# Performance work log

Hardware: AMD Instinct MI355X
Metric: run time of the kernel (lower is better)

The kernel has to match this reference:

```python
import jax, jax.numpy as jnp
import numpy as np

B, S, D, H = 4, 2048, 512, 8
EPS = 1e-5

def _layer_norm(x, gamma, beta):
    mu = jnp.mean(x, axis=-1, keepdims=True)
    var = jnp.mean(jnp.square(x - mu), axis=-1, keepdims=True)
    return (x - mu) * jax.lax.rsqrt(var + EPS) * gamma + beta

def setup_inputs() -> dict:
    key = jax.random.key(0)
    ks = jax.random.split(key, 6)
    sc = 1.0 / np.sqrt(D)
    return {
        "seq_k": jax.random.normal(ks[0], (B, S, D), jnp.float32),
        "seq_q": jax.random.normal(ks[1], (B, S, D), jnp.float32),
        "seq_v": jax.random.normal(ks[2], (B, S, D), jnp.float32),
        "W1": jax.random.normal(ks[3], (D, D), jnp.float32) * sc,
        "W2": jax.random.normal(ks[4], (D, D), jnp.float32) * sc,
        "W3": jax.random.normal(ks[5], (D, D), jnp.float32) * sc,
        "gamma": jnp.ones((D,), jnp.float32),
        "beta": jnp.zeros((D,), jnp.float32),
    }

def reference(seq_k, seq_q, seq_v, W1, W2, W3, gamma, beta):
    # is_layer_norm=True: pre-LN on values; seq_v_value is the normed v
    v_in = _layer_norm(seq_v, gamma, beta)
    # nn.Linear(bias=False): y = x @ W^T
    q = seq_q @ W1.T
    k = seq_k @ W2.T
    v = v_in @ W3.T
    hd = D // H
    q = q.reshape(B, S, H, hd).transpose(0, 2, 1, 3)  # b h s d
    k = k.reshape(B, S, H, hd).transpose(0, 2, 1, 3)
    v = v.reshape(B, S, H, hd).transpose(0, 2, 1, 3)
    # faithful quirk: scores = K @ Q^T, unscaled
    scores = jnp.einsum("bhid,bhjd->bhij", k, q)  # b h s s
    attn = jax.nn.softmax(scores, axis=-1)
    out = jnp.einsum("bhij,bhjd->bhid", attn, v)  # b h s d
    out = out.transpose(0, 2, 1, 3).reshape(B, S, D)
    out = out + v_in                 # is_residual=True
    return _layer_norm(out, gamma, beta)  # final LN
```

## Files before the change

### kernel.cpp

```cpp
#include <hip/hip_runtime.h>
#include <math.h>

#define BB 4
#define SS 2048
#define DD 512
#define HH 8
#define HD 64
#define NTOK (BB*SS)
#define EPS 1e-5f

typedef _Float16 half8v __attribute__((ext_vector_type(8)));
typedef _Float16 half4v __attribute__((ext_vector_type(4)));
typedef _Float16 half2v __attribute__((ext_vector_type(2)));
typedef float f32x4 __attribute__((ext_vector_type(4)));

__device__ __forceinline__ void gload_lds16(const void* g, void* l) {
    __builtin_amdgcn_global_load_lds(
        (const __attribute__((address_space(1))) unsigned int*)g,
        (__attribute__((address_space(3))) unsigned int*)l, 16, 0, 0);
}

__global__ __launch_bounds__(256) void ln_kernel(const float* __restrict__ x,
                                                 const float* __restrict__ res,
                                                 const float* __restrict__ gamma,
                                                 const float* __restrict__ beta,
                                                 float* __restrict__ y,
                                                 _Float16* __restrict__ y16) {
    int row = blockIdx.x;
    const float* xr = x + (size_t)row * DD;
    int t = threadIdx.x;
    float2 v = ((const float2*)xr)[t];
    if (res) {
        float2 r = ((const float2*)(res + (size_t)row * DD))[t];
        v.x += r.x; v.y += r.y;
    }
    float s = v.x + v.y;
    float ss = v.x * v.x + v.y * v.y;
    #pragma unroll
    for (int off = 32; off; off >>= 1) {
        s  += __shfl_down(s,  off);
        ss += __shfl_down(ss, off);
    }
    __shared__ float ws0[4], ws1[4];
    int wid = t >> 6, lane = t & 63;
    if (lane == 0) { ws0[wid] = s; ws1[wid] = ss; }
    __syncthreads();
    __shared__ float mu_s, rstd_s;
    if (t == 0) {
        float S0 = ws0[0] + ws0[1] + ws0[2] + ws0[3];
        float S1 = ws1[0] + ws1[1] + ws1[2] + ws1[3];
        float mu = S0 * (1.0f / DD);
        float var = S1 * (1.0f / DD) - mu * mu;
        mu_s = mu;
        rstd_s = rsqrtf(var + EPS);
    }
    __syncthreads();
    float mu = mu_s, rstd = rstd_s;
    float2 g = ((const float2*)gamma)[t];
    float2 bb = ((const float2*)beta)[t];
    float2 o;
    o.x = (v.x - mu) * rstd * g.x + bb.x;
    o.y = (v.y - mu) * rstd * g.y + bb.y;
    if (y)   ((float2*)(y + (size_t)row * DD))[t] = o;
    if (y16) {
        half2v ho; ho[0] = (_Float16)o.x; ho[1] = (_Float16)o.y;
        *(half2v*)&y16[(size_t)row * DD + 2 * t] = ho;
    }
}

__global__ __launch_bounds__(256) void cast_f2h(const float* __restrict__ src,
                                                _Float16* __restrict__ dst) {
    size_t i = ((size_t)blockIdx.x * 256 + threadIdx.x) * 4;
    float4 v = *(const float4*)(src + i);
    half4v o;
    o[0] = (_Float16)v.x; o[1] = (_Float16)v.y;
    o[2] = (_Float16)v.z; o[3] = (_Float16)v.w;
    *(half4v*)(dst + i) = o;
}

#define GBM 128
#define GBN 128
#define GBK 64
__global__ __launch_bounds__(256) void gemm_mfma(const _Float16* __restrict__ Aall,
                                                 const _Float16* __restrict__ Wall,
                                                 _Float16* __restrict__ Call) {
    __shared__ __align__(16) _Float16 As[GBM * GBK];
    __shared__ __align__(16) _Float16 Ws[GBN * GBK];
    int z = blockIdx.z;
    const _Float16* A = Aall + (size_t)z * NTOK * DD;
    const _Float16* W = Wall + (size_t)z * DD * DD;
    _Float16* C = Call + (size_t)z * NTOK * DD;
    int t = threadIdx.x, w = t >> 6, lane = t & 63, q = lane >> 4, ln = lane & 15;
    int lrow = lane >> 3, lseg = lane & 7;
    int m0 = blockIdx.y * GBM, n0 = blockIdx.x * GBN;
    int wm = w & 1, wn = w >> 1;
    f32x4 acc[4][4];
    #pragma unroll
    for (int mt = 0; mt < 4; ++mt)
        #pragma unroll
        for (int nt = 0; nt < 4; ++nt)
            acc[mt][nt] = (f32x4){0.f, 0.f, 0.f, 0.f};

    int gs = lseg ^ lrow;
    for (int k0 = 0; k0 < DD; k0 += GBK) {
        #pragma unroll
        for (int p = 0; p < 4; ++p) {
            int r = w * 32 + p * 8 + lrow;
            gload_lds16(A + (size_t)(m0 + r) * DD + k0 + gs * 8,
                        As + (size_t)(w * 32 + p * 8) * GBK);
            gload_lds16(W + (size_t)(n0 + r) * DD + k0 + gs * 8,
                        Ws + (size_t)(w * 32 + p * 8) * GBK);
        }
        __syncthreads();
        #pragma unroll
        for (int kk = 0; kk < 2; ++kk) {
            int ch = ((4 * kk + q) ^ (ln & 7)) * 8;
            half8v af[4], wf[4];
            #pragma unroll
            for (int mt = 0; mt < 4; ++mt)
                af[mt] = *(half8v*)&As[(wm * 64 + mt * 16 + ln) * GBK + ch];
            #pragma unroll
            for (int nt = 0; nt < 4; ++nt)
                wf[nt] = *(half8v*)&Ws[(wn * 64 + nt * 16 + ln) * GBK + ch];
            #pragma unroll
            for (int mt = 0; mt < 4; ++mt)
                #pragma unroll
                for (int nt = 0; nt < 4; ++nt)
                    acc[mt][nt] = __builtin_amdgcn_mfma_f32_16x16x32_f16(
                        af[mt], wf[nt], acc[mt][nt], 0, 0, 0);
        }
        __syncthreads();
    }
    #pragma unroll
    for (int mt = 0; mt < 4; ++mt) {
        int mbase = m0 + wm * 64 + mt * 16 + q * 4;
        #pragma unroll
        for (int nt = 0; nt < 4; ++nt) {
            int n = n0 + wn * 64 + nt * 16 + ln;
            int h = n >> 6, d = n & 63;
            #pragma unroll
            for (int r = 0; r < 4; ++r) {
                int m = mbase + r;
                int b = m >> 11, s = m & (SS - 1);
                C[(((size_t)(b * HH + h) * SS + s) * HD) + d] = (_Float16)acc[mt][nt][r];
            }
        }
    }
}

__global__ __launch_bounds__(256) void transpose_v(const _Float16* __restrict__ vh,
                                                   _Float16* __restrict__ vt) {
    __shared__ __align__(16) _Float16 tile[64 * 72];
    int t = threadIdx.x;
    int s0 = blockIdx.x * 64;
    int bh = blockIdx.y;
    const _Float16* src = vh + ((size_t)bh * SS) * HD;
    _Float16* dst = vt + ((size_t)bh * HD) * SS;
    #pragma unroll
    for (int p = 0; p < 2; ++p) {
        int idx = t + 256 * p;
        int r = idx >> 3, seg = idx & 7;
        *(half8v*)&tile[r * 72 + seg * 8] =
            *(const half8v*)&src[(size_t)(s0 + r) * HD + seg * 8];
    }
    __syncthreads();
    #pragma unroll
    for (int p = 0; p < 2; ++p) {
        int idx = t + 256 * p;
        int d = idx >> 3, seg = idx & 7;
        half8v o;
        #pragma unroll
        for (int e = 0; e < 8; ++e) o[e] = tile[(seg * 8 + e) * 72 + d];
        *(half8v*)&dst[(size_t)d * SS + s0 + seg * 8] = o;
    }
}

#define AI 128
#define AJ 64
#define PLD 72
__global__ __launch_bounds__(256) void attn_mfma(const _Float16* __restrict__ qh,
                                                 const _Float16* __restrict__ kh,
                                                 const _Float16* __restrict__ vt,
                                                 float* __restrict__ out) {
    __shared__ __align__(16) _Float16 Qt[AJ * HD];
    __shared__ __align__(16) _Float16 Vs[HD * AJ];
    __shared__ __align__(16) _Float16 Ps[8 * 16 * PLD];
    int t = threadIdx.x, w = t >> 6, lane = t & 63, q = lane >> 4, ln = lane & 15;
    int lrow = lane >> 3, lseg = lane & 7;
    int i0 = blockIdx.x * AI;
    int bh = blockIdx.y, b = bh >> 3, h = bh & 7;
    const _Float16* Kb = kh + (size_t)bh * SS * HD;
    const _Float16* Qb = qh + (size_t)bh * SS * HD;
    const _Float16* Vb = vt + (size_t)bh * HD * SS;

    half8v kf[2][2];
    #pragma unroll
    for (int nt = 0; nt < 2; ++nt)
        #pragma unroll
        for (int kk = 0; kk < 2; ++kk)
            kf[nt][kk] = *(const half8v*)&Kb[(size_t)(i0 + w * 32 + nt * 16 + ln) * HD
                                             + kk * 32 + q * 8];

    f32x4 oacc[4][2];
    float m_run[2], l_run[2];
    #pragma unroll
    for (int nt = 0; nt < 2; ++nt) {
        m_run[nt] = -3.0e38f;
        l_run[nt] = 0.f;
        #pragma unroll
        for (int mtd = 0; mtd < 4; ++mtd) oacc[mtd][nt] = (f32x4){0.f, 0.f, 0.f, 0.f};
    }

    int gs = lseg ^ lrow;
    for (int j0 = 0; j0 < SS; j0 += AJ) {
        #pragma unroll
        for (int p = 0; p < 2; ++p) {
            int r = w * 16 + p * 8 + lrow;
            gload_lds16(Qb + (size_t)(j0 + r) * HD + gs * 8,
                        Qt + (size_t)(w * 16 + p * 8) * HD);
            gload_lds16(Vb + (size_t)r * SS + j0 + gs * 8,
                        Vs + (size_t)(w * 16 + p * 8) * AJ);
        }
        __syncthreads();

        f32x4 sacc[4][2];
        #pragma unroll
        for (int mt = 0; mt < 4; ++mt)
            #pragma unroll
            for (int nt = 0; nt < 2; ++nt)
                sacc[mt][nt] = (f32x4){0.f, 0.f, 0.f, 0.f};
        #pragma unroll
        for (int kk = 0; kk < 2; ++kk) {
            int ch = ((4 * kk + q) ^ (ln & 7)) * 8;
            half8v qf[4];
            #pragma unroll
            for (int mt = 0; mt < 4; ++mt)
                qf[mt] = *(half8v*)&Qt[(mt * 16 + ln) * HD + ch];
            #pragma unroll
            for (int mt = 0; mt < 4; ++mt)
                #pragma unroll
                for (int nt = 0; nt < 2; ++nt)
                    sacc[mt][nt] = __builtin_amdgcn_mfma_f32_16x16x32_f16(
                        qf[mt], kf[nt][kk], sacc[mt][nt], 0, 0, 0);
        }

        #pragma unroll
        for (int nt = 0; nt < 2; ++nt) {
            float mx = -3.0e38f;
            #pragma unroll
            for (int mt = 0; mt < 4; ++mt)
                #pragma unroll
                for (int r = 0; r < 4; ++r) mx = fmaxf(mx, sacc[mt][nt][r]);
            mx = fmaxf(mx, __shfl_xor(mx, 16));
            mx = fmaxf(mx, __shfl_xor(mx, 32));
            float mo = m_run[nt];
            float mn = fmaxf(mo, mx);
            float al = __expf(mo - mn);
            m_run[nt] = mn;
            float ps = 0.f;
            #pragma unroll
            for (int mt = 0; mt < 4; ++mt) {
                half4v pv;
                #pragma unroll
                for (int r = 0; r < 4; ++r) {
                    float p = __expf(sacc[mt][nt][r] - mn);
                    ps += p;
                    pv[r] = (_Float16)p;
                }
                *(half4v*)&Ps[((size_t)(w * 2 + nt) * 16 + ln) * PLD + mt * 16 + q * 4] = pv;
            }
            ps += __shfl_xor(ps, 16);
            ps += __shfl_xor(ps, 32);
            l_run[nt] = l_run[nt] * al + ps;
            #pragma unroll
            for (int mtd = 0; mtd < 4; ++mtd) oacc[mtd][nt] *= al;
        }

        #pragma unroll
        for (int ks = 0; ks < 2; ++ks) {
            int ch = ((4 * ks + q) ^ (ln & 7)) * 8;
            half8v vf[4], pf[2];
            #pragma unroll
            for (int mtd = 0; mtd < 4; ++mtd)
                vf[mtd] = *(half8v*)&Vs[(mtd * 16 + ln) * AJ + ch];
            #pragma unroll
            for (int nt = 0; nt < 2; ++nt)
                pf[nt] = *(half8v*)&Ps[((size_t)(w * 2 + nt) * 16 + ln) * PLD + ks * 32 + q * 8];
            #pragma unroll
            for (int mtd = 0; mtd < 4; ++mtd)
                #pragma unroll
                for (int nt = 0; nt < 2; ++nt)
                    oacc[mtd][nt] = __builtin_amdgcn_mfma_f32_16x16x32_f16(
                        vf[mtd], pf[nt], oacc[mtd][nt], 0, 0, 0);
        }
        __syncthreads();
    }

    #pragma unroll
    for (int nt = 0; nt < 2; ++nt) {
        float inv = 1.0f / l_run[nt];
        int i = i0 + w * 32 + nt * 16 + ln;
        #pragma unroll
        for (int mtd = 0; mtd < 4; ++mtd) {
            float4 o;
            o.x = oacc[mtd][nt][0] * inv;
            o.y = oacc[mtd][nt][1] * inv;
            o.z = oacc[mtd][nt][2] * inv;
            o.w = oacc[mtd][nt][3] * inv;
            *(float4*)&out[(size_t)(b * SS + i) * DD + h * HD + mtd * 16 + q * 4] = o;
        }
    }
}

extern "C" void kernel_launch(void* const* d_in, const int* in_sizes, int n_in,
                              void* d_out, int out_size, void* d_ws, size_t ws_size,
                              hipStream_t stream) {
    const float* seq_k = (const float*)d_in[0];
    const float* seq_q = (const float*)d_in[1];
    const float* seq_v = (const float*)d_in[2];
    const float* W1    = (const float*)d_in[3];
    const float* W2    = (const float*)d_in[4];
    const float* W3    = (const float*)d_in[5];
    const float* gamma = (const float*)d_in[6];
    const float* beta  = (const float*)d_in[7];
    float* out = (float*)d_out;

    const size_t NE = (size_t)NTOK * DD;
    const size_t MB = 1024 * 1024;
    char* w8 = (char*)d_ws;
    float*    v_in = (float*)w8;
    _Float16* a16  = (_Float16*)(w8 + 16 * MB);
    _Float16* w16  = (_Float16*)(w8 + 40 * MB);
    _Float16* proj = (_Float16*)(w8 + 48 * MB);
    _Float16* vt   = (_Float16*)(w8 + 72 * MB);
    float*    ao   = (float*)(w8 + 16 * MB);

    _Float16* q16 = a16;
    _Float16* k16 = a16 + NE;
    _Float16* v16 = a16 + 2 * NE;
    _Float16* qh  = proj;
    _Float16* kh  = proj + NE;
    _Float16* vh  = proj + 2 * NE;

    hipLaunchKernelGGL(ln_kernel, dim3(NTOK), dim3(256), 0, stream,
                       seq_v, (const float*)nullptr, gamma, beta, v_in, v16);
    hipLaunchKernelGGL(cast_f2h, dim3(NE / 1024), dim3(256), 0, stream, seq_q, q16);
    hipLaunchKernelGGL(cast_f2h, dim3(NE / 1024), dim3(256), 0, stream, seq_k, k16);
    hipLaunchKernelGGL(cast_f2h, dim3((DD * DD) / 1024), dim3(256), 0, stream, W1, w16);
    hipLaunchKernelGGL(cast_f2h, dim3((DD * DD) / 1024), dim3(256), 0, stream, W2, w16 + (size_t)DD * DD);
    hipLaunchKernelGGL(cast_f2h, dim3((DD * DD) / 1024), dim3(256), 0, stream, W3, w16 + 2 * (size_t)DD * DD);
    hipLaunchKernelGGL(gemm_mfma, dim3(DD / GBN, NTOK / GBM, 3), dim3(256), 0, stream,
                       a16, w16, proj);
    hipLaunchKernelGGL(transpose_v, dim3(SS / 64, BB * HH), dim3(256), 0, stream, vh, vt);
    hipLaunchKernelGGL(attn_mfma, dim3(SS / AI, BB * HH), dim3(256), 0, stream,
                       qh, kh, vt, ao);
    hipLaunchKernelGGL(ln_kernel, dim3(NTOK), dim3(256), 0, stream,
                       ao, v_in, gamma, beta, out, (_Float16*)nullptr);
}
```

Baseline: 228.5 us.

## Fuse casts, write transposed V from GEMM, widen attention tile with exp2 softmax

Merges the five cast launches into two and folds log2(e) into W1 so the softmax can use exp2. The V projection GEMM now writes the transposed layout directly, which removes the separate transpose kernel, and Q/K outputs are stored as packed half4. The attention kernel doubles the key tile to 128, swizzles the LDS layouts, computes the row sum with an MFMA against a ones vector, and skips rescaling when no row maximum changes. These changes remove launches, a pass over V and some exp work, at the cost of more LDS and register pressure and slightly different rounding.

```diff
diff --git a/kernel.cpp b/kernel.cpp
--- a/kernel.cpp
+++ b/kernel.cpp
@@ -8,11 +8,33 @@
 #define HD 64
 #define NTOK (BB*SS)
 #define EPS 1e-5f
+#define NE ((size_t)NTOK * DD)
+#define WN ((size_t)DD * DD)
+#define LOG2E 1.4426950408889634f
 
 typedef _Float16 half8v __attribute__((ext_vector_type(8)));
 typedef _Float16 half4v __attribute__((ext_vector_type(4)));
 typedef _Float16 half2v __attribute__((ext_vector_type(2)));
 typedef float f32x4 __attribute__((ext_vector_type(4)));
+
+__device__ __forceinline__ float fast_exp2(float x) {
+#if __has_builtin(__builtin_amdgcn_exp2f)
+    return __builtin_amdgcn_exp2f(x);
+#else
+    return __expf(x * 0.6931471805599453f);
+#endif
+}
+
+__device__ __forceinline__ half2v pack2(float a, float b) {
+    return __builtin_bit_cast(half2v, __builtin_amdgcn_cvt_pkrtz(a, b));
+}
+
+__device__ __forceinline__ half4v pack4(float a, float b, float c, float d) {
+    half2v lo = pack2(a, b);
+    half2v hi = pack2(c, d);
+    half4v r; r[0] = lo[0]; r[1] = lo[1]; r[2] = hi[0]; r[3] = hi[1];
+    return r;
+}
 
 __device__ __forceinline__ void gload_lds16(const void* g, void* l) {
     __builtin_amdgcn_global_load_lds(
@@ -63,19 +85,30 @@
     o.y = (v.y - mu) * rstd * g.y + bb.y;
     if (y)   ((float2*)(y + (size_t)row * DD))[t] = o;
     if (y16) {
-        half2v ho; ho[0] = (_Float16)o.x; ho[1] = (_Float16)o.y;
-        *(half2v*)&y16[(size_t)row * DD + 2 * t] = ho;
-    }
-}
-
-__global__ __launch_bounds__(256) void cast_f2h(const float* __restrict__ src,
-                                                _Float16* __restrict__ dst) {
+        *(half2v*)&y16[(size_t)row * DD + 2 * t] = pack2(o.x, o.y);
+    }
+}
+
+__global__ __launch_bounds__(256) void cast_qk(const float* __restrict__ a,
+                                               const float* __restrict__ b,
+                                               _Float16* __restrict__ dst) {
     size_t i = ((size_t)blockIdx.x * 256 + threadIdx.x) * 4;
-    float4 v = *(const float4*)(src + i);
-    half4v o;
-    o[0] = (_Float16)v.x; o[1] = (_Float16)v.y;
-    o[2] = (_Float16)v.z; o[3] = (_Float16)v.w;
-    *(half4v*)(dst + i) = o;
+    const float* src = (i < NE) ? (a + i) : (b + (i - NE));
+    float4 v = *(const float4*)src;
+    *(half4v*)(dst + i) = pack4(v.x, v.y, v.z, v.w);
+}
+
+__global__ __launch_bounds__(256) void cast_w(const float* __restrict__ W1,
+                                              const float* __restrict__ W2,
+                                              const float* __restrict__ W3,
+                                              _Float16* __restrict__ dst) {
+    size_t i = ((size_t)blockIdx.x * 256 + threadIdx.x) * 4;
+    const float* src; float sc;
+    if (i < WN)            { src = W1 + i;          sc = LOG2E; }
+    else if (i < 2 * WN)   { src = W2 + (i - WN);   sc = 1.0f; }
+    else                   { src = W3 + (i - 2*WN); sc = 1.0f; }
+    float4 v = *(const float4*)src;
+    *(half4v*)(dst + i) = pack4(v.x * sc, v.y * sc, v.z * sc, v.w * sc);
 }
 
 #define GBM 128
@@ -83,13 +116,14 @@
 #define GBK 64
 __global__ __launch_bounds__(256) void gemm_mfma(const _Float16* __restrict__ Aall,
                                                  const _Float16* __restrict__ Wall,
-                                                 _Float16* __restrict__ Call) {
+                                                 _Float16* __restrict__ Call,
+                                                 _Float16* __restrict__ vtOut) {
     __shared__ __align__(16) _Float16 As[GBM * GBK];
     __shared__ __align__(16) _Float16 Ws[GBN * GBK];
     int z = blockIdx.z;
-    const _Float16* A = Aall + (size_t)z * NTOK * DD;
-    const _Float16* W = Wall + (size_t)z * DD * DD;
-    _Float16* C = Call + (size_t)z * NTOK * DD;
+    bool isv = (z == 2);
+    const _Float16* A = Aall + (size_t)z * NE;
+    const _Float16* W = Wall + (size_t)z * WN;
     int t = threadIdx.x, w = t >> 6, lane = t & 63, q = lane >> 4, ln = lane & 15;
     int lrow = lane >> 3, lseg = lane & 7;
     int m0 = blockIdx.y * GBM, n0 = blockIdx.x * GBN;
@@ -122,71 +156,66 @@
             #pragma unroll
             for (int nt = 0; nt < 4; ++nt)
                 wf[nt] = *(half8v*)&Ws[(wn * 64 + nt * 16 + ln) * GBK + ch];
-            #pragma unroll
-            for (int mt = 0; mt < 4; ++mt)
+            if (!isv) {
                 #pragma unroll
-                for (int nt = 0; nt < 4; ++nt)
-                    acc[mt][nt] = __builtin_amdgcn_mfma_f32_16x16x32_f16(
-                        af[mt], wf[nt], acc[mt][nt], 0, 0, 0);
+                for (int mt = 0; mt < 4; ++mt)
+                    #pragma unroll
+                    for (int nt = 0; nt < 4; ++nt)
+                        acc[mt][nt] = __builtin_amdgcn_mfma_f32_16x16x32_f16(
+                            wf[nt], af[mt], acc[mt][nt], 0, 0, 0);
+            } else {
+                #pragma unroll
+                for (int mt = 0; mt < 4; ++mt)
+                    #pragma unroll
+                    for (int nt = 0; nt < 4; ++nt)
+                        acc[mt][nt] = __builtin_amdgcn_mfma_f32_16x16x32_f16(
+                            af[mt], wf[nt], acc[mt][nt], 0, 0, 0);
+            }
         }
         __syncthreads();
     }
-    #pragma unroll
-    for (int mt = 0; mt < 4; ++mt) {
-        int mbase = m0 + wm * 64 + mt * 16 + q * 4;
-        #pragma unroll
-        for (int nt = 0; nt < 4; ++nt) {
-            int n = n0 + wn * 64 + nt * 16 + ln;
-            int h = n >> 6, d = n & 63;
-            #pragma unroll
-            for (int r = 0; r < 4; ++r) {
-                int m = mbase + r;
-                int b = m >> 11, s = m & (SS - 1);
-                C[(((size_t)(b * HH + h) * SS + s) * HD) + d] = (_Float16)acc[mt][nt][r];
-            }
-        }
-    }
-}
-
-__global__ __launch_bounds__(256) void transpose_v(const _Float16* __restrict__ vh,
-                                                   _Float16* __restrict__ vt) {
-    __shared__ __align__(16) _Float16 tile[64 * 72];
-    int t = threadIdx.x;
-    int s0 = blockIdx.x * 64;
-    int bh = blockIdx.y;
-    const _Float16* src = vh + ((size_t)bh * SS) * HD;
-    _Float16* dst = vt + ((size_t)bh * HD) * SS;
-    #pragma unroll
-    for (int p = 0; p < 2; ++p) {
-        int idx = t + 256 * p;
-        int r = idx >> 3, seg = idx & 7;
-        *(half8v*)&tile[r * 72 + seg * 8] =
-            *(const half8v*)&src[(size_t)(s0 + r) * HD + seg * 8];
-    }
-    __syncthreads();
-    #pragma unroll
-    for (int p = 0; p < 2; ++p) {
-        int idx = t + 256 * p;
-        int d = idx >> 3, seg = idx & 7;
-        half8v o;
-        #pragma unroll
-        for (int e = 0; e < 8; ++e) o[e] = tile[(seg * 8 + e) * 72 + d];
-        *(half8v*)&dst[(size_t)d * SS + s0 + seg * 8] = o;
+    if (!isv) {
+        _Float16* C = Call + (size_t)z * NE;
+        #pragma unroll
+        for (int mt = 0; mt < 4; ++mt) {
+            int m = m0 + wm * 64 + mt * 16 + ln;
+            int b = m >> 11, s = m & (SS - 1);
+            #pragma unroll
+            for (int nt = 0; nt < 4; ++nt) {
+                int nb = n0 + wn * 64 + nt * 16 + q * 4;
+                int h = nb >> 6, d0 = nb & 63;
+                half4v pv = pack4(acc[mt][nt][0], acc[mt][nt][1],
+                                  acc[mt][nt][2], acc[mt][nt][3]);
+                *(half4v*)&C[((size_t)(b * HH + h) * SS + s) * HD + d0] = pv;
+            }
+        }
+    } else {
+        #pragma unroll
+        for (int mt = 0; mt < 4; ++mt) {
+            int mb = m0 + wm * 64 + mt * 16 + q * 4;
+            int b = mb >> 11, s0 = mb & (SS - 1);
+            #pragma unroll
+            for (int nt = 0; nt < 4; ++nt) {
+                int n = n0 + wn * 64 + nt * 16 + ln;
+                int h = n >> 6, d = n & 63;
+                half4v pv = pack4(acc[mt][nt][0], acc[mt][nt][1],
+                                  acc[mt][nt][2], acc[mt][nt][3]);
+                *(half4v*)&vtOut[((size_t)(b * HH + h) * HD + d) * SS + s0] = pv;
+            }
+        }
     }
 }
 
 #define AI 128
-#define AJ 64
-#define PLD 72
+#define AJ 128
 __global__ __launch_bounds__(256) void attn_mfma(const _Float16* __restrict__ qh,
                                                  const _Float16* __restrict__ kh,
                                                  const _Float16* __restrict__ vt,
                                                  float* __restrict__ out) {
     __shared__ __align__(16) _Float16 Qt[AJ * HD];
     __shared__ __align__(16) _Float16 Vs[HD * AJ];
-    __shared__ __align__(16) _Float16 Ps[8 * 16 * PLD];
+    __shared__ __align__(16) _Float16 Ps[AI * AJ];
     int t = threadIdx.x, w = t >> 6, lane = t & 63, q = lane >> 4, ln = lane & 15;
-    int lrow = lane >> 3, lseg = lane & 7;
     int i0 = blockIdx.x * AI;
     int bh = blockIdx.y, b = bh >> 3, h = bh & 7;
     const _Float16* Kb = kh + (size_t)bh * SS * HD;
@@ -201,104 +230,106 @@
             kf[nt][kk] = *(const half8v*)&Kb[(size_t)(i0 + w * 32 + nt * 16 + ln) * HD
                                              + kk * 32 + q * 8];
 
-    f32x4 oacc[4][2];
-    float m_run[2], l_run[2];
+    f32x4 oacc[4][2], lacc[2];
+    float m_run[2];
     #pragma unroll
     for (int nt = 0; nt < 2; ++nt) {
         m_run[nt] = -3.0e38f;
-        l_run[nt] = 0.f;
+        lacc[nt] = (f32x4){0.f, 0.f, 0.f, 0.f};
         #pragma unroll
         for (int mtd = 0; mtd < 4; ++mtd) oacc[mtd][nt] = (f32x4){0.f, 0.f, 0.f, 0.f};
     }
-
-    int gs = lseg ^ lrow;
+    half8v ones;
+    #pragma unroll
+    for (int e = 0; e < 8; ++e) ones[e] = (_Float16)1.0f;
+    const f32x4 zf = (f32x4){0.f, 0.f, 0.f, 0.f};
+
     for (int j0 = 0; j0 < SS; j0 += AJ) {
         #pragma unroll
-        for (int p = 0; p < 2; ++p) {
-            int r = w * 16 + p * 8 + lrow;
-            gload_lds16(Qb + (size_t)(j0 + r) * HD + gs * 8,
-                        Qt + (size_t)(w * 16 + p * 8) * HD);
-            gload_lds16(Vb + (size_t)r * SS + j0 + gs * 8,
-                        Vs + (size_t)(w * 16 + p * 8) * AJ);
+        for (int p = 0; p < 4; ++p) {
+            int idx = p * 256 + t;
+            int rq = idx >> 3, cq = idx & 7;
+            gload_lds16(Qb + (size_t)(j0 + rq) * HD + (cq ^ (rq & 7)) * 8,
+                        Qt + (size_t)(p * 256 + w * 64) * 8);
+            int rv = idx >> 4, cv = idx & 15;
+            int csv = (cv & 8) | ((cv & 7) ^ (rv & 7));
+            gload_lds16(Vb + (size_t)rv * SS + j0 + csv * 8,
+                        Vs + (size_t)(p * 256 + w * 64) * 8);
         }
         __syncthreads();
 
-        f32x4 sacc[4][2];
-        #pragma unroll
-        for (int mt = 0; mt < 4; ++mt)
-            #pragma unroll
-            for (int nt = 0; nt < 2; ++nt)
-                sacc[mt][nt] = (f32x4){0.f, 0.f, 0.f, 0.f};
-        #pragma unroll
-        for (int kk = 0; kk < 2; ++kk) {
-            int ch = ((4 * kk + q) ^ (ln & 7)) * 8;
-            half8v qf[4];
-            #pragma unroll
-            for (int mt = 0; mt < 4; ++mt)
-                qf[mt] = *(half8v*)&Qt[(mt * 16 + ln) * HD + ch];
-            #pragma unroll
-            for (int mt = 0; mt < 4; ++mt)
-                #pragma unroll
-                for (int nt = 0; nt < 2; ++nt)
-                    sacc[mt][nt] = __builtin_amdgcn_mfma_f32_16x16x32_f16(
-                        qf[mt], kf[nt][kk], sacc[mt][nt], 0, 0, 0);
-        }
-
+        f32x4 sacc[8][2];
+        #pragma unroll
+        for (int mt = 0; mt < 8; ++mt) {
+            half8v qf = *(half8v*)&Qt[(mt * 16 + ln) * HD + (q ^ (ln & 7)) * 8];
+            sacc[mt][0] = __builtin_amdgcn_mfma_f32_16x16x32_f16(qf, kf[0][0], zf, 0, 0, 0);
+            sacc[mt][1] = __builtin_amdgcn_mfma_f32_16x16x32_f16(qf, kf[1][0], zf, 0, 0, 0);
+        }
+        #pragma unroll
+        for (int mt = 0; mt < 8; ++mt) {
+            half8v qf = *(half8v*)&Qt[(mt * 16 + ln) * HD + ((4 + q) ^ (ln & 7)) * 8];
+            sacc[mt][0] = __builtin_amdgcn_mfma_f32_16x16x32_f16(qf, kf[0][1], sacc[mt][0], 0, 0, 0);
+            sacc[mt][1] = __builtin_amdgcn_mfma_f32_16x16x32_f16(qf, kf[1][1], sacc[mt][1], 0, 0, 0);
+        }
+
+        float mn[2];
         #pragma unroll
         for (int nt = 0; nt < 2; ++nt) {
-            float mx = -3.0e38f;
-            #pragma unroll
-            for (int mt = 0; mt < 4; ++mt)
+            float mx = sacc[0][nt][0];
+            #pragma unroll
+            for (int mt = 0; mt < 8; ++mt)
                 #pragma unroll
                 for (int r = 0; r < 4; ++r) mx = fmaxf(mx, sacc[mt][nt][r]);
             mx = fmaxf(mx, __shfl_xor(mx, 16));
             mx = fmaxf(mx, __shfl_xor(mx, 32));
-            float mo = m_run[nt];
-            float mn = fmaxf(mo, mx);
-            float al = __expf(mo - mn);
-            m_run[nt] = mn;
-            float ps = 0.f;
-            #pragma unroll
-            for (int mt = 0; mt < 4; ++mt) {
-                half4v pv;
-                #pragma unroll
-                for (int r = 0; r < 4; ++r) {
-                    float p = __expf(sacc[mt][nt][r] - mn);
-                    ps += p;
-                    pv[r] = (_Float16)p;
-                }
-                *(half4v*)&Ps[((size_t)(w * 2 + nt) * 16 + ln) * PLD + mt * 16 + q * 4] = pv;
-            }
-            ps += __shfl_xor(ps, 16);
-            ps += __shfl_xor(ps, 32);
-            l_run[nt] = l_run[nt] * al + ps;
-            #pragma unroll
-            for (int mtd = 0; mtd < 4; ++mtd) oacc[mtd][nt] *= al;
-        }
-
-        #pragma unroll
-        for (int ks = 0; ks < 2; ++ks) {
-            int ch = ((4 * ks + q) ^ (ln & 7)) * 8;
-            half8v vf[4], pf[2];
-            #pragma unroll
-            for (int mtd = 0; mtd < 4; ++mtd)
-                vf[mtd] = *(half8v*)&Vs[(mtd * 16 + ln) * AJ + ch];
-            #pragma unroll
-            for (int nt = 0; nt < 2; ++nt)
-                pf[nt] = *(half8v*)&Ps[((size_t)(w * 2 + nt) * 16 + ln) * PLD + ks * 32 + q * 8];
-            #pragma unroll
-            for (int mtd = 0; mtd < 4; ++mtd)
-                #pragma unroll
-                for (int nt = 0; nt < 2; ++nt)
-                    oacc[mtd][nt] = __builtin_amdgcn_mfma_f32_16x16x32_f16(
-                        vf[mtd], pf[nt], oacc[mtd][nt], 0, 0, 0);
+            mn[nt] = fmaxf(m_run[nt], mx);
+        }
+        if (__any((mn[0] > m_run[0]) || (mn[1] > m_run[1]))) {
+            float a0 = fast_exp2(m_run[0] - mn[0]);
+            float a1 = fast_exp2(m_run[1] - mn[1]);
+            lacc[0] *= a0; lacc[1] *= a1;
+            #pragma unroll
+            for (int mtd = 0; mtd < 4; ++mtd) { oacc[mtd][0] *= a0; oacc[mtd][1] *= a1; }
+        }
+        m_run[0] = mn[0]; m_run[1] = mn[1];
+
+        #pragma unroll
+        for (int nt = 0; nt < 2; ++nt) {
+            int rp = w * 32 + nt * 16 + ln;
+            #pragma unroll
+            for (int mt = 0; mt < 8; ++mt) {
+                float p0 = fast_exp2(sacc[mt][nt][0] - mn[nt]);
+                float p1 = fast_exp2(sacc[mt][nt][1] - mn[nt]);
+                float p2 = fast_exp2(sacc[mt][nt][2] - mn[nt]);
+                float p3 = fast_exp2(sacc[mt][nt][3] - mn[nt]);
+                int cw = mt * 2 + (q >> 1);
+                int pos = (cw & 8) | ((cw & 7) ^ (ln & 7));
+                *(half4v*)&Ps[(size_t)rp * AJ + pos * 8 + (q & 1) * 4] =
+                    pack4(p0, p1, p2, p3);
+            }
+        }
+
+        #pragma unroll
+        for (int ks = 0; ks < 4; ++ks) {
+            int cd = ks * 4 + q;
+            int pos = ((cd & 8) | ((cd & 7) ^ (ln & 7))) * 8;
+            half8v pf0 = *(half8v*)&Ps[(size_t)(w * 32 + ln) * AJ + pos];
+            half8v pf1 = *(half8v*)&Ps[(size_t)(w * 32 + 16 + ln) * AJ + pos];
+            lacc[0] = __builtin_amdgcn_mfma_f32_16x16x32_f16(ones, pf0, lacc[0], 0, 0, 0);
+            lacc[1] = __builtin_amdgcn_mfma_f32_16x16x32_f16(ones, pf1, lacc[1], 0, 0, 0);
+            #pragma unroll
+            for (int mtd = 0; mtd < 4; ++mtd) {
+                half8v vf = *(half8v*)&Vs[(size_t)(mtd * 16 + ln) * AJ + pos];
+                oacc[mtd][0] = __builtin_amdgcn_mfma_f32_16x16x32_f16(vf, pf0, oacc[mtd][0], 0, 0, 0);
+                oacc[mtd][1] = __builtin_amdgcn_mfma_f32_16x16x32_f16(vf, pf1, oacc[mtd][1], 0, 0, 0);
+            }
         }
         __syncthreads();
     }
 
     #pragma unroll
     for (int nt = 0; nt < 2; ++nt) {
-        float inv = 1.0f / l_run[nt];
+        float inv = 1.0f / lacc[nt][0];
         int i = i0 + w * 32 + nt * 16 + ln;
         #pragma unroll
         for (int mtd = 0; mtd < 4; ++mtd) {
@@ -325,33 +356,27 @@
     const float* beta  = (const float*)d_in[7];
     float* out = (float*)d_out;
 
-    const size_t NE = (size_t)NTOK * DD;
     const size_t MB = 1024 * 1024;
     char* w8 = (char*)d_ws;
     float*    v_in = (float*)w8;
     _Float16* a16  = (_Float16*)(w8 + 16 * MB);
     _Float16* w16  = (_Float16*)(w8 + 40 * MB);
-    _Float16* proj = (_Float16*)(w8 + 48 * MB);
-    _Float16* vt   = (_Float16*)(w8 + 72 * MB);
+    _Float16* qh   = (_Float16*)(w8 + 48 * MB);
+    _Float16* vt   = (_Float16*)(w8 + 64 * MB);
     float*    ao   = (float*)(w8 + 16 * MB);
 
     _Float16* q16 = a16;
-    _Float16* k16 = a16 + NE;
     _Float16* v16 = a16 + 2 * NE;
-    _Float16* qh  = proj;
-    _Float16* kh  = proj + NE;
-    _Float16* vh  = proj + 2 * NE;
+    _Float16* kh  = qh + NE;
 
     hipLaunchKernelGGL(ln_kernel, dim3(NTOK), dim3(256), 0, stream,
                        seq_v, (const float*)nullptr, gamma, beta, v_in, v16);
-    hipLaunchKernelGGL(cast_f2h, dim3(NE / 1024), dim3(256), 0, stream, seq_q, q16);
-    hipLaunchKernelGGL(cast_f2h, dim3(NE / 1024), dim3(256), 0, stream, seq_k, k16);
-    hipLaunchKernelGGL(cast_f2h, dim3((DD * DD) / 1024), dim3(256), 0, stream, W1, w16);
-    hipLaunchKernelGGL(cast_f2h, dim3((DD * DD) / 1024), dim3(256), 0, stream, W2, w16 + (size_t)DD * DD);
-    hipLaunchKernelGGL(cast_f2h, dim3((DD * DD) / 1024), dim3(256), 0, stream, W3, w16 + 2 * (size_t)DD * DD);
+    hipLaunchKernelGGL(cast_qk, dim3((unsigned)(2 * NE / 1024)), dim3(256), 0, stream,
+                       seq_q, seq_k, q16);
+    hipLaunchKernelGGL(cast_w, dim3((unsigned)(3 * WN / 1024)), dim3(256), 0, stream,
+                       W1, W2, W3, w16);
     hipLaunchKernelGGL(gemm_mfma, dim3(DD / GBN, NTOK / GBM, 3), dim3(256), 0, stream,
-                       a16, w16, proj);
-    hipLaunchKernelGGL(transpose_v, dim3(SS / 64, BB * HH), dim3(256), 0, stream, vh, vt);
+                       a16, w16, qh, vt);
     hipLaunchKernelGGL(attn_mfma, dim3(SS / AI, BB * HH), dim3(256), 0, stream,
                        qh, kh, vt, ao);
     hipLaunchKernelGGL(ln_kernel, dim3(NTOK), dim3(256), 0, stream,
```

After: 233.4 us. 2.1% more time.
